# Kernel optimization log

Hardware: AMD Instinct MI355X
Metric: run time of the kernel (lower is better)

The kernel has to match this reference:

```python
import jax, jax.numpy as jnp
import numpy as np

N_EDGES = 8192
TOTAL_TOKENS = 2097152
OUT_CH = 128


def setup_inputs() -> dict:
    key = jax.random.key(0)
    k1, k2, k3, k4, k5 = jax.random.split(key, 5)
    overlap_similarity = jax.random.uniform(k1, (N_EDGES,), dtype=jnp.float32)
    overlap_length = jax.random.normal(k2, (N_EDGES,), dtype=jnp.float32)
    # flattened DNA tokens (A,C,G,T -> 0..3) over all edges
    tokens = jax.random.randint(k3, (TOTAL_TOKENS,), 0, 4, dtype=jnp.int32)
    # sorted segment ids -> ragged variable-length reads per edge
    segment_ids = jnp.sort(jax.random.randint(k4, (TOTAL_TOKENS,), 0, N_EDGES, dtype=jnp.int32))
    embedding = jax.random.normal(k5, (4, OUT_CH), dtype=jnp.float32)
    return {
        "overlap_similarity": overlap_similarity,
        "overlap_length": overlap_length,
        "tokens": tokens,
        "segment_ids": segment_ids,
        "embedding": embedding,
        "n_edges": N_EDGES,
    }


def reference(overlap_similarity, overlap_length, tokens, segment_ids, embedding, n_edges):
    # Ragged embedding-bag mean: for each edge, mean of embedding[tokens] over its read.
    # (overlap_similarity / overlap_length are unused by the original forward's output.)
    embeds = embedding[tokens]  # [T, D]
    sums = jax.ops.segment_sum(embeds, segment_ids, num_segments=n_edges)  # [E, D]
    counts = jax.ops.segment_sum(
        jnp.ones((tokens.shape[0],), dtype=embeds.dtype), segment_ids, num_segments=n_edges
    )  # [E]
    return sums / jnp.maximum(counts, 1.0)[:, None]
```

## Files before the change

### kernel.cpp

```cpp
#include <hip/hip_runtime.h>

#define OUT_CH 128
#define TOK_PER_THREAD 32

__global__ void edge_hist_kernel(const int* __restrict__ tokens,
                                 const int* __restrict__ segids,
                                 unsigned long long* __restrict__ hist,
                                 int total_tokens) {
    int tid = blockIdx.x * blockDim.x + threadIdx.x;
    long base = (long)tid * TOK_PER_THREAD;
    if (base >= total_tokens) return;

    int cur = -1;
    unsigned long long acc = 0;

    if (base + TOK_PER_THREAD <= total_tokens) {
        const int4* tok4 = (const int4*)(tokens + base);
        const int4* seg4 = (const int4*)(segids + base);
#pragma unroll
        for (int i = 0; i < TOK_PER_THREAD / 4; ++i) {
            int4 t = tok4[i];
            int4 s = seg4[i];
            int tt[4] = {t.x, t.y, t.z, t.w};
            int ss[4] = {s.x, s.y, s.z, s.w};
#pragma unroll
            for (int j = 0; j < 4; ++j) {
                if (ss[j] != cur) {
                    if (acc) atomicAdd(&hist[cur], acc);
                    cur = ss[j];
                    acc = 0;
                }
                acc += 1ull << (tt[j] << 4);
            }
        }
    } else {
        for (long k = base; k < total_tokens; ++k) {
            int s = segids[k];
            int t = tokens[k];
            if (s != cur) {
                if (acc) atomicAdd(&hist[cur], acc);
                cur = s;
                acc = 0;
            }
            acc += 1ull << (t << 4);
        }
    }
    if (acc) atomicAdd(&hist[cur], acc);
}

__global__ void edge_out_kernel(const unsigned long long* __restrict__ hist,
                                const float* __restrict__ emb,
                                float* __restrict__ out,
                                int n_edges) {
    int tid = blockIdx.x * blockDim.x + threadIdx.x;
    int e = tid >> 5;
    int c = (tid & 31) << 2;
    if (e >= n_edges) return;

    unsigned long long h = hist[e];
    float c0 = (float)(h & 0xFFFFull);
    float c1 = (float)((h >> 16) & 0xFFFFull);
    float c2 = (float)((h >> 32) & 0xFFFFull);
    float c3 = (float)((h >> 48) & 0xFFFFull);
    float tot = c0 + c1 + c2 + c3;
    float inv = 1.0f / fmaxf(tot, 1.0f);

    const float4 e0 = *(const float4*)(emb + 0 * OUT_CH + c);
    const float4 e1 = *(const float4*)(emb + 1 * OUT_CH + c);
    const float4 e2 = *(const float4*)(emb + 2 * OUT_CH + c);
    const float4 e3 = *(const float4*)(emb + 3 * OUT_CH + c);

    float4 r;
    r.x = (c0 * e0.x + c1 * e1.x + c2 * e2.x + c3 * e3.x) * inv;
    r.y = (c0 * e0.y + c1 * e1.y + c2 * e2.y + c3 * e3.y) * inv;
    r.z = (c0 * e0.z + c1 * e1.z + c2 * e2.z + c3 * e3.z) * inv;
    r.w = (c0 * e0.w + c1 * e1.w + c2 * e2.w + c3 * e3.w) * inv;

    *(float4*)(out + (long)e * OUT_CH + c) = r;
}

extern "C" void kernel_launch(void* const* d_in, const int* in_sizes, int n_in,
                              void* d_out, int out_size, void* d_ws, size_t ws_size,
                              hipStream_t stream) {
    const int* tokens = (const int*)d_in[2];
    const int* segids = (const int*)d_in[3];
    const float* emb  = (const float*)d_in[4];
    float* out = (float*)d_out;

    const int T = in_sizes[2];
    const int n_edges = out_size / OUT_CH;

    unsigned long long* hist = (unsigned long long*)d_ws;

    hipMemsetAsync(hist, 0, (size_t)n_edges * sizeof(unsigned long long), stream);

    int threads1 = (T + TOK_PER_THREAD - 1) / TOK_PER_THREAD;
    int blocks1 = (threads1 + 255) / 256;
    edge_hist_kernel<<<blocks1, 256, 0, stream>>>(tokens, segids, hist, T);

    int threads2 = n_edges * (OUT_CH / 4);
    int blocks2 = (threads2 + 255) / 256;
    edge_out_kernel<<<blocks2, 256, 0, stream>>>(hist, emb, out, n_edges);
}
```

Before: 89.28 us.

## Fuse histogram and output into one wave-per-edge kernel with binary search

Replaces the memset, atomic histogram kernel and output kernel with a single kernel where each wavefront owns one edge. The wave binary-searches the sorted segment ids to find its token range, counts tokens with packed 16-bit counters and a shuffle reduction, then writes the mean embedding row. This removes the segment-id stream read, the global atomics and two extra launches. In exchange each wave makes about 21 dependent global loads for the search, and token loads are scalar rather than vectorized.

```diff
diff --git a/kernel.cpp b/kernel.cpp
--- a/kernel.cpp
+++ b/kernel.cpp
@@ -1,82 +1,57 @@
 #include <hip/hip_runtime.h>
 
 #define OUT_CH 128
-#define TOK_PER_THREAD 32
+#define WAVES_PER_BLOCK 4
 
-__global__ void edge_hist_kernel(const int* __restrict__ tokens,
-                                 const int* __restrict__ segids,
-                                 unsigned long long* __restrict__ hist,
-                                 int total_tokens) {
-    int tid = blockIdx.x * blockDim.x + threadIdx.x;
-    long base = (long)tid * TOK_PER_THREAD;
-    if (base >= total_tokens) return;
+__global__ __launch_bounds__(WAVES_PER_BLOCK * 64)
+void edge_fused_kernel(const int* __restrict__ tokens,
+                       const int* __restrict__ segids,
+                       const float* __restrict__ emb,
+                       float* __restrict__ out,
+                       int T, int E) {
+    const int lane = threadIdx.x & 63;
+    const int wid  = threadIdx.x >> 6;
+    const int e = blockIdx.x * WAVES_PER_BLOCK + wid;
+    if (e >= E) return;
 
-    int cur = -1;
+    int lo0 = 0, hi0 = T;
+    int lo1 = 0, hi1 = T;
+    while ((lo0 < hi0) | (lo1 < hi1)) {
+        int mid0 = (lo0 + hi0) >> 1;
+        int mid1 = (lo1 + hi1) >> 1;
+        int v0 = (lo0 < hi0) ? segids[mid0] : 0x7FFFFFFF;
+        int v1 = (lo1 < hi1) ? segids[mid1] : 0x7FFFFFFF;
+        if (lo0 < hi0) { if (v0 < e)     lo0 = mid0 + 1; else hi0 = mid0; }
+        if (lo1 < hi1) { if (v1 < e + 1) lo1 = mid1 + 1; else hi1 = mid1; }
+    }
+    const int start = lo0, end = lo1;
+
     unsigned long long acc = 0;
+    for (int k = start + lane; k < end; k += 64) {
+        acc += 1ull << (tokens[k] << 4);
+    }
+    #pragma unroll
+    for (int m = 32; m > 0; m >>= 1) {
+        acc += __shfl_xor(acc, m, 64);
+    }
 
-    if (base + TOK_PER_THREAD <= total_tokens) {
-        const int4* tok4 = (const int4*)(tokens + base);
-        const int4* seg4 = (const int4*)(segids + base);
-#pragma unroll
-        for (int i = 0; i < TOK_PER_THREAD / 4; ++i) {
-            int4 t = tok4[i];
-            int4 s = seg4[i];
-            int tt[4] = {t.x, t.y, t.z, t.w};
-            int ss[4] = {s.x, s.y, s.z, s.w};
-#pragma unroll
-            for (int j = 0; j < 4; ++j) {
-                if (ss[j] != cur) {
-                    if (acc) atomicAdd(&hist[cur], acc);
-                    cur = ss[j];
-                    acc = 0;
-                }
-                acc += 1ull << (tt[j] << 4);
-            }
-        }
-    } else {
-        for (long k = base; k < total_tokens; ++k) {
-            int s = segids[k];
-            int t = tokens[k];
-            if (s != cur) {
-                if (acc) atomicAdd(&hist[cur], acc);
-                cur = s;
-                acc = 0;
-            }
-            acc += 1ull << (t << 4);
-        }
-    }
-    if (acc) atomicAdd(&hist[cur], acc);
-}
+    const float c0 = (float)(acc & 0xFFFFull);
+    const float c1 = (float)((acc >> 16) & 0xFFFFull);
+    const float c2 = (float)((acc >> 32) & 0xFFFFull);
+    const float c3 = (float)((acc >> 48) & 0xFFFFull);
+    const float tot = c0 + c1 + c2 + c3;
+    const float inv = 1.0f / fmaxf(tot, 1.0f);
 
-__global__ void edge_out_kernel(const unsigned long long* __restrict__ hist,
-                                const float* __restrict__ emb,
-                                float* __restrict__ out,
-                                int n_edges) {
-    int tid = blockIdx.x * blockDim.x + threadIdx.x;
-    int e = tid >> 5;
-    int c = (tid & 31) << 2;
-    if (e >= n_edges) return;
+    const int c = lane << 1;
+    const float2 e0 = *(const float2*)(emb + 0 * OUT_CH + c);
+    const float2 e1 = *(const float2*)(emb + 1 * OUT_CH + c);
+    const float2 e2 = *(const float2*)(emb + 2 * OUT_CH + c);
+    const float2 e3 = *(const float2*)(emb + 3 * OUT_CH + c);
 
-    unsigned long long h = hist[e];
-    float c0 = (float)(h & 0xFFFFull);
-    float c1 = (float)((h >> 16) & 0xFFFFull);
-    float c2 = (float)((h >> 32) & 0xFFFFull);
-    float c3 = (float)((h >> 48) & 0xFFFFull);
-    float tot = c0 + c1 + c2 + c3;
-    float inv = 1.0f / fmaxf(tot, 1.0f);
-
-    const float4 e0 = *(const float4*)(emb + 0 * OUT_CH + c);
-    const float4 e1 = *(const float4*)(emb + 1 * OUT_CH + c);
-    const float4 e2 = *(const float4*)(emb + 2 * OUT_CH + c);
-    const float4 e3 = *(const float4*)(emb + 3 * OUT_CH + c);
-
-    float4 r;
+    float2 r;
     r.x = (c0 * e0.x + c1 * e1.x + c2 * e2.x + c3 * e3.x) * inv;
     r.y = (c0 * e0.y + c1 * e1.y + c2 * e2.y + c3 * e3.y) * inv;
-    r.z = (c0 * e0.z + c1 * e1.z + c2 * e2.z + c3 * e3.z) * inv;
-    r.w = (c0 * e0.w + c1 * e1.w + c2 * e2.w + c3 * e3.w) * inv;
-
-    *(float4*)(out + (long)e * OUT_CH + c) = r;
+    *(float2*)(out + (size_t)e * OUT_CH + c) = r;
 }
 
 extern "C" void kernel_launch(void* const* d_in, const int* in_sizes, int n_in,
@@ -88,17 +63,9 @@
     float* out = (float*)d_out;
 
     const int T = in_sizes[2];
-    const int n_edges = out_size / OUT_CH;
+    const int E = out_size / OUT_CH;
 
-    unsigned long long* hist = (unsigned long long*)d_ws;
-
-    hipMemsetAsync(hist, 0, (size_t)n_edges * sizeof(unsigned long long), stream);
-
-    int threads1 = (T + TOK_PER_THREAD - 1) / TOK_PER_THREAD;
-    int blocks1 = (threads1 + 255) / 256;
-    edge_hist_kernel<<<blocks1, 256, 0, stream>>>(tokens, segids, hist, T);
-
-    int threads2 = n_edges * (OUT_CH / 4);
-    int blocks2 = (threads2 + 255) / 256;
-    edge_out_kernel<<<blocks2, 256, 0, stream>>>(hist, emb, out, n_edges);
+    const int blocks = (E + WAVES_PER_BLOCK - 1) / WAVES_PER_BLOCK;
+    edge_fused_kernel<<<blocks, WAVES_PER_BLOCK * 64, 0, stream>>>(
+        tokens, segids, emb, out, T, E);
 }
```

Result: slower. 91.90 us (+2.9%).
